# Performance work log

Measured on AMD Instinct MI355X. Metric: run time of the kernel, lower is better.

Reference implementation:

```python
import jax, jax.numpy as jnp
import numpy as np

B, T, D, HS = 8, 2048, 1024, 64


def setup_inputs() -> dict:
    key = jax.random.key(0)
    ks = jax.random.split(key, 7)
    return {
        "x": jax.random.normal(ks[0], (B, T, D), dtype=jnp.float32),
        "Wq": jax.random.normal(ks[1], (D, HS), dtype=jnp.float32) / np.sqrt(D),
        "bq": jax.random.normal(ks[2], (HS,), dtype=jnp.float32) * 0.01,
        "Wk": jax.random.normal(ks[3], (D, HS), dtype=jnp.float32) / np.sqrt(D),
        "bk": jax.random.normal(ks[4], (HS,), dtype=jnp.float32) * 0.01,
        "Wv": jax.random.normal(ks[5], (D, HS), dtype=jnp.float32) / np.sqrt(D),
        "bv": jax.random.normal(ks[6], (HS,), dtype=jnp.float32) * 0.01,
    }


def reference(x, Wq, bq, Wk, bk, Wv, bv):
    # Q,K,V projections: [B,T,D] @ [D,HS] -> [B,T,HS]
    Q = x @ Wq + bq
    K = x @ Wk + bk
    V = x @ Wv + bv
    # raw scores [B,T,T]
    scores = jnp.einsum("bqh,bkh->bqk", Q, K)
    # causal mask applied BEFORE scaling (as in the original; -inf is scale-invariant)
    causal = jnp.tril(jnp.ones((T, T), dtype=bool))
    scores = jnp.where(causal[None, :, :], scores, -jnp.inf)
    scores = scores / jnp.sqrt(jnp.asarray(HS, dtype=scores.dtype))
    attn = jax.nn.softmax(scores, axis=-1)
    # dropout is identity in eval mode (deterministic reference)
    return jnp.einsum("bqk,bkh->bqh", attn, V)
```

## Files before the change

### kernel.cpp

```cpp
#include <hip/hip_runtime.h>
#include <hip/hip_bf16.h>

typedef __bf16 bf16x8 __attribute__((ext_vector_type(8)));
typedef __bf16 bf16x4 __attribute__((ext_vector_type(4)));
typedef float  f32x4  __attribute__((ext_vector_type(4)));

#define B_  8
#define T_  2048
#define D_  1024
#define HS_ 64


__global__ __launch_bounds__(256) void pack_w(
    const float* __restrict__ Wq, const float* __restrict__ Wk,
    const float* __restrict__ Wv, __bf16* __restrict__ Wp)
{
    const int t    = blockIdx.x * 256 + threadIdx.x;
    const int lane = t & 63;
    const int pg   = t >> 6;
    const int s    = pg & 3;
    const int c    = (pg >> 2) & 31;
    const int p    = pg >> 7;
    const int m16  = lane & 15;
    const int quad = lane >> 4;

    const float* W = (p == 0) ? Wq : (p == 1) ? Wk : Wv;
    const float* src = W + (size_t)(c * 32 + quad * 8) * 64 + s * 16 + m16;
    bf16x8 frag;
    #pragma unroll
    for (int j = 0; j < 8; ++j) frag[j] = (__bf16)src[(size_t)j * 64];
    *(bf16x8*)(Wp + (size_t)pg * 512 + lane * 8) = frag;
}

__global__ __launch_bounds__(256) void qkv_fused(
    const float* __restrict__ x,
    const __bf16* __restrict__ Wp,
    const float* __restrict__ bq, const float* __restrict__ bk,
    const float* __restrict__ bv,
    __bf16* __restrict__ Q, __bf16* __restrict__ K, __bf16* __restrict__ Vt)
{
    __shared__ alignas(16) unsigned char Smem[36864];

    const int rt   = blockIdx.x;
    const int wave = threadIdx.x >> 6;
    const int lane = threadIdx.x & 63;
    const int m16  = lane & 15;
    const int quad = lane >> 4;
    const int row0 = rt * 16;

    __bf16* Xs = (__bf16*)(Smem + wave * 8448);

    {
        const float* xsrc = x + (size_t)row0 * 1024 + wave * 256;
        const int sr = lane >> 5;
        const int sc = (lane & 31) * 8;
        #pragma unroll
        for (int i = 0; i < 8; ++i) {
            const int r = i * 2 + sr;
            f32x4 v0 = *(const f32x4*)(xsrc + (size_t)r * 1024 + sc);
            f32x4 v1 = *(const f32x4*)(xsrc + (size_t)r * 1024 + sc + 4);
            bf16x8 w;
            #pragma unroll
            for (int e = 0; e < 4; ++e) { w[e] = (__bf16)v0[e]; w[4 + e] = (__bf16)v1[e]; }
            *(bf16x8*)&Xs[r * 264 + sc] = w;
        }
    }
    __builtin_amdgcn_wave_barrier();

    f32x4 acc[3][4];
    #pragma unroll
    for (int p = 0; p < 3; ++p)
        #pragma unroll
        for (int s = 0; s < 4; ++s) acc[p][s] = {0.f, 0.f, 0.f, 0.f};

    for (int k0 = 0; k0 < 256; k0 += 32) {
        bf16x8 a = *(const bf16x8*)&Xs[m16 * 264 + k0 + quad * 8];
        const int cbase = wave * 8 + (k0 >> 5);

        bf16x8 bf[12];
        #pragma unroll
        for (int ps = 0; ps < 12; ++ps) {
            const int p = ps >> 2, s = ps & 3;
            bf[ps] = *(const bf16x8*)(Wp +
                ((size_t)((p * 32 + cbase) * 4 + s) << 9) + lane * 8);
        }
        __builtin_amdgcn_sched_barrier(0);

        #pragma unroll
        for (int ps = 0; ps < 12; ++ps)
            acc[ps >> 2][ps & 3] =
                __builtin_amdgcn_mfma_f32_16x16x32_bf16(a, bf[ps], acc[ps >> 2][ps & 3], 0, 0, 0);
    }

    f32x4* Red = (f32x4*)Smem;
    __syncthreads();
    if (wave != 0) {
        #pragma unroll
        for (int p = 0; p < 3; ++p)
            #pragma unroll
            for (int s = 0; s < 4; ++s)
                Red[((wave - 1) * 12 + p * 4 + s) * 64 + lane] = acc[p][s];
    }
    __syncthreads();
    if (wave != 0) return;

    #pragma unroll
    for (int p = 0; p < 3; ++p)
        #pragma unroll
        for (int s = 0; s < 4; ++s) {
            f32x4 sum = acc[p][s];
            #pragma unroll
            for (int w = 0; w < 3; ++w) {
                f32x4 v = Red[(w * 12 + p * 4 + s) * 64 + lane];
                #pragma unroll
                for (int e = 0; e < 4; ++e) sum[e] += v[e];
            }
            acc[p][s] = sum;
        }

    #pragma unroll
    for (int s = 0; s < 4; ++s) {
        const int h = s * 16 + m16;
        const float bia = bq[h];
        #pragma unroll
        for (int r = 0; r < 4; ++r)
            Q[(size_t)(row0 + quad * 4 + r) * 64 + h] = (__bf16)(acc[0][s][r] + bia);
    }
    #pragma unroll
    for (int s = 0; s < 4; ++s) {
        const int h = s * 16 + m16;
        const float bia = bk[h];
        #pragma unroll
        for (int r = 0; r < 4; ++r)
            K[(size_t)(row0 + quad * 4 + r) * 64 + h] = (__bf16)(acc[1][s][r] + bia);
    }
    {
        const int bidx = row0 >> 11;
        const int t0   = (row0 & 2047) + quad * 4;
        #pragma unroll
        for (int s = 0; s < 4; ++s) {
            const int h = s * 16 + m16;
            const float bia = bv[h];
            bf16x4 pack;
            #pragma unroll
            for (int r = 0; r < 4; ++r) pack[r] = (__bf16)(acc[2][s][r] + bia);
            *(bf16x4*)(Vt + (size_t)bidx * (HS_ * T_) + (size_t)h * T_ + t0) = pack;
        }
    }
}

__global__ __launch_bounds__(256) void attn_partial(
    const __bf16* __restrict__ Q,
    const __bf16* __restrict__ K,
    const __bf16* __restrict__ Vt,
    float* __restrict__ Opart,
    float* __restrict__ Ml)
{
    __shared__ alignas(16) __bf16 Klds[8 * 512];
    __shared__ alignas(16) __bf16 Vlds[8 * 512];

    const int z  = blockIdx.x;
    const int qt = blockIdx.y;
    const int b  = blockIdx.z;
    if (z > qt) return;

    const int tid  = threadIdx.x;
    const int wave = tid >> 6;
    const int lane = tid & 63;
    const int m16  = lane & 15;
    const int quad = lane >> 4;

    const __bf16* Qb = Q  + (size_t)b * T_ * HS_;
    const __bf16* Kb = K  + (size_t)b * T_ * HS_;
    const __bf16* Vb = Vt + (size_t)b * HS_ * T_;

    const int q0   = qt * 64 + wave * 16;
    const int qrow = q0 + m16;

    bf16x8 qb0 = *(const bf16x8*)(Qb + (size_t)qrow * 64 + quad * 8);
    bf16x8 qb1 = *(const bf16x8*)(Qb + (size_t)qrow * 64 + 32 + quad * 8);

    f32x4 o[4];
    #pragma unroll
    for (int hs = 0; hs < 4; ++hs) o[hs] = {0.f, 0.f, 0.f, 0.f};
    float m_run = -1e30f, l_run = 0.f;

    for (int jt = z; jt <= qt; jt += 8) {
        const int j0 = jt * 64;

        #pragma unroll
        for (int i = 0; i < 2; ++i) {
            const int p    = i * 256 + tid;
            const int trow = p >> 3;
            const int tcol = p & 7;
            bf16x8 kv = *(const bf16x8*)(Kb + (size_t)(j0 + trow) * 64 + tcol * 8);
            const int snb = ((trow >> 5) << 1) | ((trow >> 2) & 1);
            const int mk  = (((trow >> 3) & 3) << 2) | (trow & 3);
            *(bf16x8*)&Klds[((((snb << 1) | (tcol >> 2)) << 6) + (tcol & 3) * 16 + mk) * 8] = kv;
            bf16x8 vv = *(const bf16x8*)(Vb + (size_t)trow * T_ + j0 + tcol * 8);
            *(bf16x8*)&Vlds[(((((trow >> 4) << 1) | (tcol >> 2)) << 6) + (tcol & 3) * 16 + (trow & 15)) * 8] = vv;
        }
        __syncthreads();

        f32x4 s[4];
        #pragma unroll
        for (int snb = 0; snb < 4; ++snb) s[snb] = {0.f, 0.f, 0.f, 0.f};
        #pragma unroll
        for (int snb = 0; snb < 4; ++snb) {
            bf16x8 ka0 = *(const bf16x8*)&Klds[((snb * 2 + 0) * 64 + lane) * 8];
            bf16x8 ka1 = *(const bf16x8*)&Klds[((snb * 2 + 1) * 64 + lane) * 8];
            s[snb] = __builtin_amdgcn_mfma_f32_16x16x32_bf16(ka0, qb0, s[snb], 0, 0, 0);
            s[snb] = __builtin_amdgcn_mfma_f32_16x16x32_bf16(ka1, qb1, s[snb], 0, 0, 0);
        }

        float mx = -1e30f;
        #pragma unroll
        for (int snb = 0; snb < 4; ++snb) {
            const int kbase = j0 + ((snb >> 1) << 5) + (quad << 3) + ((snb & 1) << 2);
            #pragma unroll
            for (int r = 0; r < 4; ++r) {
                float v = s[snb][r] * 0.125f;
                v = (kbase + r <= qrow) ? v : -1e30f;
                s[snb][r] = v;
                mx = fmaxf(mx, v);
            }
        }
        mx = fmaxf(mx, __shfl_xor(mx, 16));
        mx = fmaxf(mx, __shfl_xor(mx, 32));

        const float newm  = fmaxf(m_run, mx);
        const float alpha = __expf(m_run - newm);
        m_run = newm;

        float rs = 0.f;
        #pragma unroll
        for (int snb = 0; snb < 4; ++snb)
            #pragma unroll
            for (int r = 0; r < 4; ++r) {
                float pv = __expf(s[snb][r] - newm);
                s[snb][r] = pv;
                rs += pv;
            }
        rs += __shfl_xor(rs, 16);
        rs += __shfl_xor(rs, 32);
        l_run = l_run * alpha + rs;

        #pragma unroll
        for (int hs = 0; hs < 4; ++hs)
            #pragma unroll
            for (int r = 0; r < 4; ++r) o[hs][r] *= alpha;

        bf16x8 pb0, pb1;
        #pragma unroll
        for (int r = 0; r < 4; ++r) {
            pb0[r]     = (__bf16)s[0][r];
            pb0[4 + r] = (__bf16)s[1][r];
            pb1[r]     = (__bf16)s[2][r];
            pb1[4 + r] = (__bf16)s[3][r];
        }

        #pragma unroll
        for (int hs = 0; hs < 4; ++hs) {
            bf16x8 va0 = *(const bf16x8*)&Vlds[((hs * 2 + 0) * 64 + lane) * 8];
            bf16x8 va1 = *(const bf16x8*)&Vlds[((hs * 2 + 1) * 64 + lane) * 8];
            o[hs] = __builtin_amdgcn_mfma_f32_16x16x32_bf16(va0, pb0, o[hs], 0, 0, 0);
            o[hs] = __builtin_amdgcn_mfma_f32_16x16x32_bf16(va1, pb1, o[hs], 0, 0, 0);
        }
        __syncthreads();
    }

    const int slot = (b * 32 + qt) * 8 + z;
    float* Op = Opart + (size_t)slot * 4096;
    #pragma unroll
    for (int hs = 0; hs < 4; ++hs)
        *(f32x4*)(Op + (size_t)(wave * 16 + m16) * 64 + hs * 16 + quad * 4) = o[hs];
    if (quad == 0) {
        Ml[(size_t)slot * 128 + (wave * 16 + m16) * 2 + 0] = m_run;
        Ml[(size_t)slot * 128 + (wave * 16 + m16) * 2 + 1] = l_run;
    }
}

__global__ __launch_bounds__(256) void attn_merge(
    const float* __restrict__ Opart, const float* __restrict__ Ml,
    float* __restrict__ O)
{
    const int qt = blockIdx.x;
    const int b  = blockIdx.y;
    const int tid = threadIdx.x;
    const int row = tid >> 2;
    const int colblk = tid & 3;
    const int nc = (qt + 1 < 8) ? qt + 1 : 8;
    const int slotBase = (b * 32 + qt) * 8;

    f32x4 acc[4];
    #pragma unroll
    for (int j = 0; j < 4; ++j) acc[j] = {0.f, 0.f, 0.f, 0.f};
    float M = -1e30f, den = 0.f;

    for (int c = 0; c < nc; ++c) {
        const float* mlp = Ml + (size_t)(slotBase + c) * 128 + row * 2;
        const float mc = mlp[0];
        const float lc = mlp[1];
        const float newM  = fmaxf(M, mc);
        const float alpha = __expf(M - newM);
        const float w     = __expf(mc - newM);
        M = newM;

        const float* op = Opart + (size_t)(slotBase + c) * 4096 + row * 64 + colblk * 16;
        #pragma unroll
        for (int j = 0; j < 4; ++j) {
            f32x4 v = *(const f32x4*)(op + j * 4);
            #pragma unroll
            for (int e = 0; e < 4; ++e) acc[j][e] = acc[j][e] * alpha + w * v[e];
        }
        den = den * alpha + w * lc;
    }

    const float inv = 1.f / den;
    float* out = O + ((size_t)b * T_ + qt * 64 + row) * 64 + colblk * 16;
    #pragma unroll
    for (int j = 0; j < 4; ++j) {
        f32x4 v;
        #pragma unroll
        for (int e = 0; e < 4; ++e) v[e] = acc[j][e] * inv;
        *(f32x4*)(out + j * 4) = v;
    }
}

extern "C" void kernel_launch(void* const* d_in, const int* in_sizes, int n_in,
                              void* d_out, int out_size, void* d_ws, size_t ws_size,
                              hipStream_t stream)
{
    const float* x  = (const float*)d_in[0];
    const float* Wq = (const float*)d_in[1];
    const float* bq = (const float*)d_in[2];
    const float* Wk = (const float*)d_in[3];
    const float* bk = (const float*)d_in[4];
    const float* Wv = (const float*)d_in[5];
    const float* bv = (const float*)d_in[6];
    float* out = (float*)d_out;

    __bf16* Wp = (__bf16*)d_ws;
    __bf16* Q  = Wp + 384 * 512;
    __bf16* K  = Q  + (size_t)B_ * T_ * HS_;
    __bf16* Vt = K  + (size_t)B_ * T_ * HS_;
    float* Opart = (float*)(Vt + (size_t)B_ * T_ * HS_);
    float* Ml    = Opart + (size_t)2048 * 4096;

    pack_w<<<96, 256, 0, stream>>>(Wq, Wk, Wv, Wp);
    qkv_fused<<<1024, 256, 0, stream>>>(x, Wp, bq, bk, bv, Q, K, Vt);
    attn_partial<<<dim3(8, 32, 8), 256, 0, stream>>>(Q, K, Vt, Opart, Ml);
    attn_merge<<<dim3(32, 8), 256, 0, stream>>>(Opart, Ml, out);
}
```

Measured before the change: 148.4 us.

## Load K/V fragments directly from global memory and parallelize split-K merge

The attention kernel no longer stages K and V tiles through shared memory with two block barriers per iteration. Each wave now loads its MFMA operand fragments straight from global memory into registers, relying on L2/L1 to serve the reloads across the four waves. The merge kernel is rewritten to load all split statistics up front, compute a global max and scale factors, and accumulate with twice as many blocks and narrower per-thread columns. The trade-off is four times redundant global/cache traffic for K/V and more register pressure, in exchange for removing LDS stores and synchronization.

Measured after the change: 174.7 us. 1.18x slower.

```diff
diff --git a/kernel.cpp b/kernel.cpp
--- a/kernel.cpp
+++ b/kernel.cpp
@@ -156,9 +156,6 @@
     float* __restrict__ Opart,
     float* __restrict__ Ml)
 {
-    __shared__ alignas(16) __bf16 Klds[8 * 512];
-    __shared__ alignas(16) __bf16 Vlds[8 * 512];
-
     const int z  = blockIdx.x;
     const int qt = blockIdx.y;
     const int b  = blockIdx.z;
@@ -180,6 +177,17 @@
     bf16x8 qb0 = *(const bf16x8*)(Qb + (size_t)qrow * 64 + quad * 8);
     bf16x8 qb1 = *(const bf16x8*)(Qb + (size_t)qrow * 64 + 32 + quad * 8);
 
+    const __bf16* kf[4];
+    #pragma unroll
+    for (int snb = 0; snb < 4; ++snb) {
+        const int key = ((snb >> 1) << 5) + ((m16 >> 2) << 3) + ((snb & 1) << 2) + (m16 & 3);
+        kf[snb] = Kb + (size_t)key * 64 + quad * 8;
+    }
+    const __bf16* vf[4];
+    #pragma unroll
+    for (int hs = 0; hs < 4; ++hs)
+        vf[hs] = Vb + (size_t)(hs * 16 + m16) * T_ + quad * 8;
+
     f32x4 o[4];
     #pragma unroll
     for (int hs = 0; hs < 4; ++hs) o[hs] = {0.f, 0.f, 0.f, 0.f};
@@ -187,30 +195,27 @@
 
     for (int jt = z; jt <= qt; jt += 8) {
         const int j0 = jt * 64;
-
-        #pragma unroll
-        for (int i = 0; i < 2; ++i) {
-            const int p    = i * 256 + tid;
-            const int trow = p >> 3;
-            const int tcol = p & 7;
-            bf16x8 kv = *(const bf16x8*)(Kb + (size_t)(j0 + trow) * 64 + tcol * 8);
-            const int snb = ((trow >> 5) << 1) | ((trow >> 2) & 1);
-            const int mk  = (((trow >> 3) & 3) << 2) | (trow & 3);
-            *(bf16x8*)&Klds[((((snb << 1) | (tcol >> 2)) << 6) + (tcol & 3) * 16 + mk) * 8] = kv;
-            bf16x8 vv = *(const bf16x8*)(Vb + (size_t)trow * T_ + j0 + tcol * 8);
-            *(bf16x8*)&Vlds[(((((trow >> 4) << 1) | (tcol >> 2)) << 6) + (tcol & 3) * 16 + (trow & 15)) * 8] = vv;
-        }
-        __syncthreads();
+        const size_t kofs = (size_t)j0 * 64;
+
+        bf16x8 ka0[4], ka1[4], va0[4], va1[4];
+        #pragma unroll
+        for (int snb = 0; snb < 4; ++snb) {
+            ka0[snb] = *(const bf16x8*)(kf[snb] + kofs);
+            ka1[snb] = *(const bf16x8*)(kf[snb] + kofs + 32);
+        }
+        #pragma unroll
+        for (int hs = 0; hs < 4; ++hs) {
+            va0[hs] = *(const bf16x8*)(vf[hs] + j0);
+            va1[hs] = *(const bf16x8*)(vf[hs] + j0 + 32);
+        }
 
         f32x4 s[4];
         #pragma unroll
         for (int snb = 0; snb < 4; ++snb) s[snb] = {0.f, 0.f, 0.f, 0.f};
         #pragma unroll
         for (int snb = 0; snb < 4; ++snb) {
-            bf16x8 ka0 = *(const bf16x8*)&Klds[((snb * 2 + 0) * 64 + lane) * 8];
-            bf16x8 ka1 = *(const bf16x8*)&Klds[((snb * 2 + 1) * 64 + lane) * 8];
-            s[snb] = __builtin_amdgcn_mfma_f32_16x16x32_bf16(ka0, qb0, s[snb], 0, 0, 0);
-            s[snb] = __builtin_amdgcn_mfma_f32_16x16x32_bf16(ka1, qb1, s[snb], 0, 0, 0);
+            s[snb] = __builtin_amdgcn_mfma_f32_16x16x32_bf16(ka0[snb], qb0, s[snb], 0, 0, 0);
+            s[snb] = __builtin_amdgcn_mfma_f32_16x16x32_bf16(ka1[snb], qb1, s[snb], 0, 0, 0);
         }
 
         float mx = -1e30f;
@@ -261,12 +266,9 @@
 
         #pragma unroll
         for (int hs = 0; hs < 4; ++hs) {
-            bf16x8 va0 = *(const bf16x8*)&Vlds[((hs * 2 + 0) * 64 + lane) * 8];
-            bf16x8 va1 = *(const bf16x8*)&Vlds[((hs * 2 + 1) * 64 + lane) * 8];
-            o[hs] = __builtin_amdgcn_mfma_f32_16x16x32_bf16(va0, pb0, o[hs], 0, 0, 0);
-            o[hs] = __builtin_amdgcn_mfma_f32_16x16x32_bf16(va1, pb1, o[hs], 0, 0, 0);
-        }
-        __syncthreads();
+            o[hs] = __builtin_amdgcn_mfma_f32_16x16x32_bf16(va0[hs], pb0, o[hs], 0, 0, 0);
+            o[hs] = __builtin_amdgcn_mfma_f32_16x16x32_bf16(va1[hs], pb1, o[hs], 0, 0, 0);
+        }
     }
 
     const int slot = (b * 32 + qt) * 8 + z;
@@ -284,47 +286,50 @@
     const float* __restrict__ Opart, const float* __restrict__ Ml,
     float* __restrict__ O)
 {
-    const int qt = blockIdx.x;
-    const int b  = blockIdx.y;
+    const int qt  = blockIdx.x >> 1;
+    const int rh  = blockIdx.x & 1;
+    const int b   = blockIdx.y;
     const int tid = threadIdx.x;
-    const int row = tid >> 2;
-    const int colblk = tid & 3;
-    const int nc = (qt + 1 < 8) ? qt + 1 : 8;
+    const int row = rh * 32 + (tid >> 3);
+    const int cb  = tid & 7;
+    const int nc  = (qt + 1 < 8) ? qt + 1 : 8;
     const int slotBase = (b * 32 + qt) * 8;
 
-    f32x4 acc[4];
-    #pragma unroll
-    for (int j = 0; j < 4; ++j) acc[j] = {0.f, 0.f, 0.f, 0.f};
-    float M = -1e30f, den = 0.f;
-
-    for (int c = 0; c < nc; ++c) {
-        const float* mlp = Ml + (size_t)(slotBase + c) * 128 + row * 2;
-        const float mc = mlp[0];
-        const float lc = mlp[1];
-        const float newM  = fmaxf(M, mc);
-        const float alpha = __expf(M - newM);
-        const float w     = __expf(mc - newM);
-        M = newM;
-
-        const float* op = Opart + (size_t)(slotBase + c) * 4096 + row * 64 + colblk * 16;
-        #pragma unroll
-        for (int j = 0; j < 4; ++j) {
-            f32x4 v = *(const f32x4*)(op + j * 4);
-            #pragma unroll
-            for (int e = 0; e < 4; ++e) acc[j][e] = acc[j][e] * alpha + w * v[e];
-        }
-        den = den * alpha + w * lc;
-    }
-
+    float m[8], l[8], sc[8];
+    #pragma unroll
+    for (int c = 0; c < 8; ++c) {
+        const int cc = (c < nc) ? c : nc - 1;
+        const float* mlp = Ml + (size_t)(slotBase + cc) * 128 + row * 2;
+        m[c] = mlp[0];
+        l[c] = (c < nc) ? mlp[1] : 0.f;
+    }
+    float M = m[0];
+    #pragma unroll
+    for (int c = 1; c < 8; ++c) M = fmaxf(M, m[c]);
+    float den = 0.f;
+    #pragma unroll
+    for (int c = 0; c < 8; ++c) {
+        sc[c] = (c < nc) ? __expf(m[c] - M) : 0.f;
+        den += sc[c] * l[c];
+    }
     const float inv = 1.f / den;
-    float* out = O + ((size_t)b * T_ + qt * 64 + row) * 64 + colblk * 16;
-    #pragma unroll
-    for (int j = 0; j < 4; ++j) {
-        f32x4 v;
-        #pragma unroll
-        for (int e = 0; e < 4; ++e) v[e] = acc[j][e] * inv;
-        *(f32x4*)(out + j * 4) = v;
-    }
+    #pragma unroll
+    for (int c = 0; c < 8; ++c) sc[c] *= inv;
+
+    f32x4 a0 = {0.f, 0.f, 0.f, 0.f}, a1 = {0.f, 0.f, 0.f, 0.f};
+    #pragma unroll
+    for (int c = 0; c < 8; ++c) {
+        const int cc = (c < nc) ? c : nc - 1;
+        const float* op = Opart + (size_t)(slotBase + cc) * 4096 + row * 64 + cb * 8;
+        f32x4 v0 = *(const f32x4*)op;
+        f32x4 v1 = *(const f32x4*)(op + 4);
+        #pragma unroll
+        for (int e = 0; e < 4; ++e) { a0[e] += sc[c] * v0[e]; a1[e] += sc[c] * v1[e]; }
+    }
+
+    float* out = O + ((size_t)b * T_ + qt * 64 + row) * 64 + cb * 8;
+    *(f32x4*)out       = a0;
+    *(f32x4*)(out + 4) = a1;
 }
 
 extern "C" void kernel_launch(void* const* d_in, const int* in_sizes, int n_in,
@@ -350,5 +355,5 @@
     pack_w<<<96, 256, 0, stream>>>(Wq, Wk, Wv, Wp);
     qkv_fused<<<1024, 256, 0, stream>>>(x, Wp, bq, bk, bv, Q, K, Vt);
     attn_partial<<<dim3(8, 32, 8), 256, 0, stream>>>(Q, K, Vt, Opart, Ml);
-    attn_merge<<<dim3(32, 8), 256, 0, stream>>>(Opart, Ml, out);
-}
+    attn_merge<<<dim3(64, 8), 256, 0, stream>>>(Opart, Ml, out);
+}
```

## Replace split-KV partial+merge attention with single fused kernel and register prefetch

Applied to the files above, without the earlier changes.

Removes the split-KV decomposition and the separate merge kernel: each block now processes all causal KV tiles for one query tile and writes normalized output directly. The next K/V tile is prefetched into registers while the current one is computed. This removes partial-output and statistics traffic and one launch, but reduces parallelism to 256 blocks with heavily imbalanced causal work, lengthening the critical path.

Measured after the change: 158.2 us. +6.6%, slower.

```diff
diff --git a/kernel.cpp b/kernel.cpp
--- a/kernel.cpp
+++ b/kernel.cpp
@@ -149,20 +149,17 @@
     }
 }
 
-__global__ __launch_bounds__(256) void attn_partial(
+__global__ __launch_bounds__(256) void attn_fused(
     const __bf16* __restrict__ Q,
     const __bf16* __restrict__ K,
     const __bf16* __restrict__ Vt,
-    float* __restrict__ Opart,
-    float* __restrict__ Ml)
+    float* __restrict__ O)
 {
     __shared__ alignas(16) __bf16 Klds[8 * 512];
     __shared__ alignas(16) __bf16 Vlds[8 * 512];
 
-    const int z  = blockIdx.x;
-    const int qt = blockIdx.y;
-    const int b  = blockIdx.z;
-    if (z > qt) return;
+    const int qt = blockIdx.x;
+    const int b  = blockIdx.y;
 
     const int tid  = threadIdx.x;
     const int wave = tid >> 6;
@@ -180,27 +177,50 @@
     bf16x8 qb0 = *(const bf16x8*)(Qb + (size_t)qrow * 64 + quad * 8);
     bf16x8 qb1 = *(const bf16x8*)(Qb + (size_t)qrow * 64 + 32 + quad * 8);
 
+    int koffL[2], voffL[2];
+    const __bf16* kgb[2];
+    const __bf16* vgb[2];
+    #pragma unroll
+    for (int i = 0; i < 2; ++i) {
+        const int p    = i * 256 + tid;
+        const int trow = p >> 3;
+        const int tcol = p & 7;
+        const int snb  = ((trow >> 5) << 1) | ((trow >> 2) & 1);
+        const int mk   = (((trow >> 3) & 3) << 2) | (trow & 3);
+        koffL[i] = ((((snb << 1) | (tcol >> 2)) << 6) + (tcol & 3) * 16 + mk) * 8;
+        voffL[i] = (((((trow >> 4) << 1) | (tcol >> 2)) << 6) + (tcol & 3) * 16 + (trow & 15)) * 8;
+        kgb[i] = Kb + (size_t)trow * 64 + tcol * 8;
+        vgb[i] = Vb + (size_t)trow * T_ + tcol * 8;
+    }
+
     f32x4 o[4];
     #pragma unroll
     for (int hs = 0; hs < 4; ++hs) o[hs] = {0.f, 0.f, 0.f, 0.f};
     float m_run = -1e30f, l_run = 0.f;
 
-    for (int jt = z; jt <= qt; jt += 8) {
+    bf16x8 kr0 = *(const bf16x8*)(kgb[0]);
+    bf16x8 kr1 = *(const bf16x8*)(kgb[1]);
+    bf16x8 vr0 = *(const bf16x8*)(vgb[0]);
+    bf16x8 vr1 = *(const bf16x8*)(vgb[1]);
+
+    for (int jt = 0; jt <= qt; ++jt) {
         const int j0 = jt * 64;
 
-        #pragma unroll
-        for (int i = 0; i < 2; ++i) {
-            const int p    = i * 256 + tid;
-            const int trow = p >> 3;
-            const int tcol = p & 7;
-            bf16x8 kv = *(const bf16x8*)(Kb + (size_t)(j0 + trow) * 64 + tcol * 8);
-            const int snb = ((trow >> 5) << 1) | ((trow >> 2) & 1);
-            const int mk  = (((trow >> 3) & 3) << 2) | (trow & 3);
-            *(bf16x8*)&Klds[((((snb << 1) | (tcol >> 2)) << 6) + (tcol & 3) * 16 + mk) * 8] = kv;
-            bf16x8 vv = *(const bf16x8*)(Vb + (size_t)trow * T_ + j0 + tcol * 8);
-            *(bf16x8*)&Vlds[(((((trow >> 4) << 1) | (tcol >> 2)) << 6) + (tcol & 3) * 16 + (trow & 15)) * 8] = vv;
-        }
         __syncthreads();
+        *(bf16x8*)&Klds[koffL[0]] = kr0;
+        *(bf16x8*)&Klds[koffL[1]] = kr1;
+        *(bf16x8*)&Vlds[voffL[0]] = vr0;
+        *(bf16x8*)&Vlds[voffL[1]] = vr1;
+        __syncthreads();
+
+        if (jt < qt) {
+            const size_t nk = (size_t)(j0 + 64) * 64;
+            kr0 = *(const bf16x8*)(kgb[0] + nk);
+            kr1 = *(const bf16x8*)(kgb[1] + nk);
+            vr0 = *(const bf16x8*)(vgb[0] + j0 + 64);
+            vr1 = *(const bf16x8*)(vgb[1] + j0 + 64);
+        }
+        __builtin_amdgcn_sched_barrier(0);
 
         f32x4 s[4];
         #pragma unroll
@@ -266,64 +286,16 @@
             o[hs] = __builtin_amdgcn_mfma_f32_16x16x32_bf16(va0, pb0, o[hs], 0, 0, 0);
             o[hs] = __builtin_amdgcn_mfma_f32_16x16x32_bf16(va1, pb1, o[hs], 0, 0, 0);
         }
-        __syncthreads();
-    }
-
-    const int slot = (b * 32 + qt) * 8 + z;
-    float* Op = Opart + (size_t)slot * 4096;
-    #pragma unroll
-    for (int hs = 0; hs < 4; ++hs)
-        *(f32x4*)(Op + (size_t)(wave * 16 + m16) * 64 + hs * 16 + quad * 4) = o[hs];
-    if (quad == 0) {
-        Ml[(size_t)slot * 128 + (wave * 16 + m16) * 2 + 0] = m_run;
-        Ml[(size_t)slot * 128 + (wave * 16 + m16) * 2 + 1] = l_run;
-    }
-}
-
-__global__ __launch_bounds__(256) void attn_merge(
-    const float* __restrict__ Opart, const float* __restrict__ Ml,
-    float* __restrict__ O)
-{
-    const int qt = blockIdx.x;
-    const int b  = blockIdx.y;
-    const int tid = threadIdx.x;
-    const int row = tid >> 2;
-    const int colblk = tid & 3;
-    const int nc = (qt + 1 < 8) ? qt + 1 : 8;
-    const int slotBase = (b * 32 + qt) * 8;
-
-    f32x4 acc[4];
-    #pragma unroll
-    for (int j = 0; j < 4; ++j) acc[j] = {0.f, 0.f, 0.f, 0.f};
-    float M = -1e30f, den = 0.f;
-
-    for (int c = 0; c < nc; ++c) {
-        const float* mlp = Ml + (size_t)(slotBase + c) * 128 + row * 2;
-        const float mc = mlp[0];
-        const float lc = mlp[1];
-        const float newM  = fmaxf(M, mc);
-        const float alpha = __expf(M - newM);
-        const float w     = __expf(mc - newM);
-        M = newM;
-
-        const float* op = Opart + (size_t)(slotBase + c) * 4096 + row * 64 + colblk * 16;
-        #pragma unroll
-        for (int j = 0; j < 4; ++j) {
-            f32x4 v = *(const f32x4*)(op + j * 4);
-            #pragma unroll
-            for (int e = 0; e < 4; ++e) acc[j][e] = acc[j][e] * alpha + w * v[e];
-        }
-        den = den * alpha + w * lc;
-    }
-
-    const float inv = 1.f / den;
-    float* out = O + ((size_t)b * T_ + qt * 64 + row) * 64 + colblk * 16;
-    #pragma unroll
-    for (int j = 0; j < 4; ++j) {
+    }
+
+    const float inv = 1.f / l_run;
+    float* Ob = O + ((size_t)b * T_ + (size_t)(qt * 64 + wave * 16 + m16)) * 64;
+    #pragma unroll
+    for (int hs = 0; hs < 4; ++hs) {
         f32x4 v;
         #pragma unroll
-        for (int e = 0; e < 4; ++e) v[e] = acc[j][e] * inv;
-        *(f32x4*)(out + j * 4) = v;
+        for (int r = 0; r < 4; ++r) v[r] = o[hs][r] * inv;
+        *(f32x4*)(Ob + hs * 16 + quad * 4) = v;
     }
 }
 
@@ -344,11 +316,8 @@
     __bf16* Q  = Wp + 384 * 512;
     __bf16* K  = Q  + (size_t)B_ * T_ * HS_;
     __bf16* Vt = K  + (size_t)B_ * T_ * HS_;
-    float* Opart = (float*)(Vt + (size_t)B_ * T_ * HS_);
-    float* Ml    = Opart + (size_t)2048 * 4096;
 
     pack_w<<<96, 256, 0, stream>>>(Wq, Wk, Wv, Wp);
     qkv_fused<<<1024, 256, 0, stream>>>(x, Wp, bq, bk, bv, Q, K, Vt);
-    attn_partial<<<dim3(8, 32, 8), 256, 0, stream>>>(Q, K, Vt, Opart, Ml);
-    attn_merge<<<dim3(32, 8), 256, 0, stream>>>(Opart, Ml, out);
+    attn_fused<<<dim3(32, 8), 256, 0, stream>>>(Q, K, Vt, out);
 }
```
